# Optimization experiments

Hardware: AMD Instinct MI355X
Metric: run time of the kernel (lower is better)

Reference implementation:

```python
import jax, jax.numpy as jnp
import numpy as np

N_Q = 10000
B, S = 128, 200
M = 50          # memory_size
DK = 64         # memory_key_state_dim == q_embed_dim == final_fc_dim
DV = 128        # memory_value_state_dim == qa_embed_dim
F = 64          # final_fc_dim


def setup_inputs() -> dict:
    key = jax.random.key(0)
    ks = jax.random.split(key, 14)
    q_data = jax.random.randint(ks[0], (B, S), 0, N_Q + 1)
    qa_data = jax.random.randint(ks[1], (B, S), 0, 2 * N_Q + 1)
    # target in {-1 (pad), 0, 1}
    target = jax.random.randint(ks[2], (B, S), -1, 2).astype(jnp.float32)
    q_embed_w = jax.random.normal(ks[3], (N_Q + 1, DK), jnp.float32) * 0.1
    q_embed_w = q_embed_w.at[0].set(0.0)  # padding_idx=0
    qa_embed_w = jax.random.normal(ks[4], (2 * N_Q + 1, DV), jnp.float32) * 0.1
    qa_embed_w = qa_embed_w.at[0].set(0.0)
    mem_key = jax.random.normal(ks[5], (M, DK), jnp.float32) * (2.0 / DK) ** 0.5
    init_mem_value = jax.random.normal(ks[6], (M, DV), jnp.float32) * (2.0 / DV) ** 0.5
    erase_w = jax.random.normal(ks[7], (DV, DV), jnp.float32) * (2.0 / DV) ** 0.5
    erase_b = jnp.zeros((DV,), jnp.float32)
    add_w = jax.random.normal(ks[8], (DV, DV), jnp.float32) * (2.0 / DV) ** 0.5
    add_b = jnp.zeros((DV,), jnp.float32)
    read_w = jax.random.normal(ks[9], (F, DV + F), jnp.float32) * (2.0 / (DV + F)) ** 0.5
    read_b = jnp.zeros((F,), jnp.float32)
    pred_w = jax.random.normal(ks[10], (1, F), jnp.float32) * (2.0 / F) ** 0.5
    pred_b = jnp.zeros((1,), jnp.float32)
    return {
        'q_data': q_data, 'qa_data': qa_data, 'target': target,
        'q_embed_w': q_embed_w, 'qa_embed_w': qa_embed_w,
        'mem_key': mem_key, 'init_mem_value': init_mem_value,
        'erase_w': erase_w, 'erase_b': erase_b,
        'add_w': add_w, 'add_b': add_b,
        'read_w': read_w, 'read_b': read_b,
        'pred_w': pred_w, 'pred_b': pred_b,
    }


def reference(q_data, qa_data, target, q_embed_w, qa_embed_w, mem_key,
              init_mem_value, erase_w, erase_b, add_w, add_b,
              read_w, read_b, pred_w, pred_b):
    q_e = q_embed_w[q_data]    # [B,S,DK]
    qa_e = qa_embed_w[qa_data]  # [B,S,DV]
    Mv0 = jnp.broadcast_to(init_mem_value, (q_data.shape[0],) + init_mem_value.shape)  # [B,M,DV]

    def step(Mv, x):
        q, qa = x                                           # [B,DK], [B,DV]
        w = jax.nn.softmax(q @ mem_key.T, axis=1)           # addressing -> [B,M]
        read = jnp.einsum('bm,bmv->bv', w, Mv)              # weighted read (before write)
        e = jax.nn.sigmoid(qa @ erase_w.T + erase_b)        # [B,DV]
        a = jnp.tanh(qa @ add_w.T + add_b)                  # [B,DV]
        Mv_new = Mv * (1.0 - w[:, :, None] * e[:, None, :]) + w[:, :, None] * a[:, None, :]
        return Mv_new, read

    _, reads = jax.lax.scan(step, Mv0, (q_e.transpose(1, 0, 2), qa_e.transpose(1, 0, 2)))
    reads = reads.transpose(1, 0, 2)                        # [B,S,DV]

    h = jnp.tanh(jnp.concatenate([reads, q_e], axis=-1) @ read_w.T + read_b)  # [B,S,F]
    logits = (h @ pred_w.T + pred_b)[..., 0]                # [B,S]

    mask = target >= 0
    t = jnp.where(mask, target, 0.0)
    # stable BCE with logits
    bce = jnp.maximum(logits, 0.0) - logits * t + jnp.log1p(jnp.exp(-jnp.abs(logits)))
    n_valid = jnp.maximum(jnp.sum(mask.astype(jnp.float32)), 1.0)
    loss = jnp.sum(jnp.where(mask, bce, 0.0)) / n_valid
    probs = jnp.where(mask, jax.nn.sigmoid(logits), 0.0)    # masked predictions, fixed shape
    return loss, probs
```

## Files before the change

kernel.cpp:

```cpp
#include <hip/hip_runtime.h>
#include <math.h>

#define BB 128
#define SS 200
#define MM 50
#define DKK 64
#define DVV 128
#define FF 64
#define NROW (BB*SS)

#define WROW 64
#define NFCB (NROW/64)
#define WLDS 136
#define FLDS 200
#define CLEN 25
#define MP 25
#define NSCB 100

#define W_OFF   0L
#define EA_OFF  (W_OFF + (long)NROW*WROW)
#define R_OFF   (EA_OFF + (long)NROW*DVV*2)
#define ACC_OFF (R_OFF + (long)NROW*DVV)

typedef __attribute__((ext_vector_type(8))) short bf16x8;
typedef __attribute__((ext_vector_type(4))) float f32x4;
typedef __attribute__((ext_vector_type(2))) float f32x2;

__device__ __forceinline__ short f2bf(float f) {
    unsigned u = __builtin_bit_cast(unsigned, f);
    u += 0x7fff + ((u >> 16) & 1);
    return (short)(u >> 16);
}
__device__ __forceinline__ bf16x8 cvt8(const float* p) {
    float4 lo = *(const float4*)p;
    float4 hi = *(const float4*)(p + 4);
    bf16x8 f;
    f[0] = f2bf(lo.x); f[1] = f2bf(lo.y); f[2] = f2bf(lo.z); f[3] = f2bf(lo.w);
    f[4] = f2bf(hi.x); f[5] = f2bf(hi.y); f[6] = f2bf(hi.z); f[7] = f2bf(hi.w);
    return f;
}

__global__ __launch_bounds__(256) void k_pre(const int* __restrict__ q_data,
                                             const float* __restrict__ q_embed_w,
                                             const float* __restrict__ mem_key,
                                             const int* __restrict__ qa_data,
                                             const float* __restrict__ qa_embed_w,
                                             const float* __restrict__ erase_w,
                                             const float* __restrict__ erase_b,
                                             const float* __restrict__ add_w,
                                             const float* __restrict__ add_b,
                                             float* __restrict__ w_out,
                                             float* __restrict__ EA,
                                             float* __restrict__ acc) {
    __shared__ union {
        short  wl[2 * 128 * WLDS];
        float4 mk[MM * 16];
    } sh;
    int tid = threadIdx.x;
    int bid = blockIdx.x;

    if (bid < NSCB) {
        if (bid == 0 && tid == 0) {
            acc[0] = 0.f; acc[1] = 0.f;
            ((unsigned*)acc)[2] = 0u;
        }
        const float4* mkg = (const float4*)mem_key;
        for (int i = tid; i < MM * 16; i += 256) sh.mk[i] = mkg[i];
        __syncthreads();

        int item = bid * 256 + tid;
        int qidx = q_data[item];
        const float4* qg = (const float4*)(q_embed_w + (long)qidx * DKK);
        float4 q[16];
#pragma unroll
        for (int i = 0; i < 16; i++) q[i] = qg[i];

        float s[MM];
        float mx = -1e30f;
#pragma unroll 2
        for (int m = 0; m < MM; m++) {
            float a = 0.f;
#pragma unroll
            for (int k4 = 0; k4 < 16; k4++) {
                float4 mkv = sh.mk[m * 16 + k4];
                float4 qv = q[k4];
                a = fmaf(qv.x, mkv.x, a);
                a = fmaf(qv.y, mkv.y, a);
                a = fmaf(qv.z, mkv.z, a);
                a = fmaf(qv.w, mkv.w, a);
            }
            s[m] = a;
            mx = fmaxf(mx, a);
        }
        float sum = 0.f;
#pragma unroll
        for (int m = 0; m < MM; m++) { s[m] = expf(s[m] - mx); sum += s[m]; }
        float inv = 1.f / sum;

        float* wo = w_out + (long)item * WROW;
#pragma unroll
        for (int m = 0; m < MM; m++) wo[m] = s[m] * inv;
#pragma unroll
        for (int m = MM; m < WROW; m++) wo[m] = 0.f;
        return;
    }

    int r0 = (bid - NSCB) * 64;
    int lane = tid & 63;
    int wv = tid >> 6;
    int n = lane & 15;
    int quad = lane >> 4;

    for (int i = tid; i < 8192; i += 256) {
        int mat = i >> 12;
        int r = (i >> 5) & 127;
        int p = i & 31;
        float4 src = *(const float4*)((mat ? add_w : erase_w) + r * 128 + p * 4);
        short4 d;
        d.x = f2bf(src.x); d.y = f2bf(src.y); d.z = f2bf(src.z); d.w = f2bf(src.w);
        *(short4*)(sh.wl + (mat * 128 + r) * WLDS + p * 4) = d;
    }

    int arow = r0 + wv * 16 + n;
    int qidx = qa_data[arow];
    const float* qp = qa_embed_w + (long)qidx * DVV + quad * 8;
    bf16x8 afrag[4];
#pragma unroll
    for (int kb = 0; kb < 4; kb++) afrag[kb] = cvt8(qp + kb * 32);

    float eb_[8], ab_[8];
#pragma unroll
    for (int vt = 0; vt < 8; vt++) {
        eb_[vt] = erase_b[vt * 16 + n];
        ab_[vt] = add_b[vt * 16 + n];
    }
    __syncthreads();

    int rowbase = r0 + wv * 16 + quad * 4;
#pragma unroll 2
    for (int vt = 0; vt < 8; vt++) {
        int vrow = vt * 16 + n;
        f32x4 ae = {0.f, 0.f, 0.f, 0.f};
        f32x4 aa = {0.f, 0.f, 0.f, 0.f};
#pragma unroll
        for (int kb = 0; kb < 4; kb++) {
            bf16x8 be = *(const bf16x8*)(sh.wl + vrow * WLDS + kb * 32 + quad * 8);
            bf16x8 ba = *(const bf16x8*)(sh.wl + (128 + vrow) * WLDS + kb * 32 + quad * 8);
            ae = __builtin_amdgcn_mfma_f32_16x16x32_bf16(afrag[kb], be, ae, 0, 0, 0);
            aa = __builtin_amdgcn_mfma_f32_16x16x32_bf16(afrag[kb], ba, aa, 0, 0, 0);
        }
        int v = vt * 16 + n;
        float eb = eb_[vt], ab = ab_[vt];
#pragma unroll
        for (int r = 0; r < 4; r++) {
            float ev = 1.f / (1.f + __expf(-(ae[r] + eb)));
            float av = 2.f / (1.f + __expf(-2.f * (aa[r] + ab))) - 1.f;
            float2 o; o.x = ev; o.y = av;
            *(float2*)(EA + (((long)(rowbase + r)) * DVV + v) * 2) = o;
        }
    }
}

__device__ __forceinline__ void scan_pass1(const float4* __restrict__ wq,
                                           const float* __restrict__ eab,
                                           f32x2* A2, f32x2* B2) {
    const f32x2 one = {1.f, 1.f};
    float2 e0 = *(const float2*)eab;
    float2 e1 = *(const float2*)(eab + (long)1 * DVV * 2);
#pragma unroll 1
    for (int t = 0; t < CLEN; t++) {
        int tp = (t + 2 < CLEN) ? t + 2 : CLEN - 1;
        float2 en = *(const float2*)(eab + (long)tp * DVV * 2);
        f32x2 ne2 = {-e0.x, -e0.x};
        f32x2 a2  = {e0.y, e0.y};
#pragma unroll
        for (int c = 0; c < 13; c++) {
            float4 q = wq[t * 16 + c];
            {
                int j = 2 * c;
                f32x2 w2 = {q.x, q.y};
                f32x2 al = w2 * ne2 + one;
                A2[j] = A2[j] * al;
                B2[j] = al * B2[j] + w2 * a2;
            }
            if (c < 12) {
                int j = 2 * c + 1;
                f32x2 w2 = {q.z, q.w};
                f32x2 al = w2 * ne2 + one;
                A2[j] = A2[j] * al;
                B2[j] = al * B2[j] + w2 * a2;
            }
        }
        e0 = e1; e1 = en;
    }
}

__device__ __forceinline__ void scan_pass2(const float4* __restrict__ wq,
                                           const float* __restrict__ eab,
                                           float* __restrict__ Rb,
                                           f32x2* Mv) {
    float2 e0 = *(const float2*)eab;
    float2 e1 = *(const float2*)(eab + (long)1 * DVV * 2);
#pragma unroll 1
    for (int t = 0; t < CLEN; t++) {
        int tp = (t + 2 < CLEN) ? t + 2 : CLEN - 1;
        float2 en = *(const float2*)(eab + (long)tp * DVV * 2);
        f32x2 ne2 = {-e0.x, -e0.x};
        f32x2 a2  = {e0.y, e0.y};
        f32x2 rd  = {0.f, 0.f};
#pragma unroll
        for (int c = 0; c < 13; c++) {
            float4 q = wq[t * 16 + c];
            {
                int j = 2 * c;
                f32x2 w2 = {q.x, q.y};
                rd = rd + w2 * Mv[j];
                f32x2 s = ne2 * Mv[j] + a2;
                Mv[j] = Mv[j] + w2 * s;
            }
            if (c < 12) {
                int j = 2 * c + 1;
                f32x2 w2 = {q.z, q.w};
                rd = rd + w2 * Mv[j];
                f32x2 s = ne2 * Mv[j] + a2;
                Mv[j] = Mv[j] + w2 * s;
            }
        }
        Rb[t * DVV] = rd.x + rd.y;
        e0 = e1; e1 = en;
    }
}

__global__ __launch_bounds__(512, 1) void k_scan(const float* __restrict__ w_pad,
                                                 const float* __restrict__ EA,
                                                 const float* __restrict__ init_mv,
                                                 float* __restrict__ R) {
    __shared__ float Wl[SS * WROW];
    __shared__ float Sb[MM * 64];
    int b   = blockIdx.x >> 1;
    int vh  = blockIdx.x & 1;
    int tid = threadIdx.x;
    int lane  = tid & 63;
    int chunk = tid >> 6;
    int v  = vh * 64 + lane;
    int t0 = chunk * CLEN;

    {
        const float4* wg = (const float4*)(w_pad + (long)b * SS * WROW);
        float4* wl4 = (float4*)Wl;
        for (int i = tid; i < SS * WROW / 4; i += 512) wl4[i] = wg[i];
    }
    __syncthreads();

    const float4* wq  = (const float4*)(Wl + t0 * WROW);
    const float*  eab = EA + (((long)b * SS + t0) * DVV + v) * 2;
    float*        Rb  = R + ((long)b * SS + t0) * DVV + v;

    const f32x2 one = {1.f, 1.f};
    f32x2 A2[MP], B2[MP];
    f32x2 Mv[MP];

    if (chunk == 0) {
#pragma unroll
        for (int j = 0; j < MP; j++) {
            Mv[j].x = init_mv[(2 * j) * DVV + v];
            Mv[j].y = init_mv[(2 * j + 1) * DVV + v];
        }
        scan_pass2(wq, eab, Rb, Mv);
#pragma unroll
        for (int j = 0; j < MP; j++) {
            Sb[(2 * j) * 64 + lane] = Mv[j].x;
            Sb[(2 * j + 1) * 64 + lane] = Mv[j].y;
        }
    } else if (chunk < 7) {
#pragma unroll
        for (int j = 0; j < MP; j++) { A2[j] = one; B2[j] = (f32x2){0.f, 0.f}; }
        scan_pass1(wq, eab, A2, B2);
    }
    __syncthreads();

    for (int c = 1; c < 8; c++) {
        if (chunk == c) {
#pragma unroll
            for (int j = 0; j < MP; j++) {
                Mv[j].x = Sb[(2 * j) * 64 + lane];
                Mv[j].y = Sb[(2 * j + 1) * 64 + lane];
            }
            if (c < 7) {
#pragma unroll
                for (int j = 0; j < MP; j++) {
                    f32x2 nb = A2[j] * Mv[j] + B2[j];
                    Sb[(2 * j) * 64 + lane] = nb.x;
                    Sb[(2 * j + 1) * 64 + lane] = nb.y;
                }
            }
        }
        __syncthreads();
    }

    if (chunk > 0) scan_pass2(wq, eab, Rb, Mv);
}

__global__ __launch_bounds__(256) void k_fc(const float* __restrict__ Rr,
                                            const int* __restrict__ q_data,
                                            const float* __restrict__ q_embed_w,
                                            const float* __restrict__ read_w,
                                            const float* __restrict__ read_b,
                                            const float* __restrict__ pred_w,
                                            const float* __restrict__ pred_b,
                                            const float* __restrict__ target,
                                            float* __restrict__ out,
                                            float* __restrict__ acc) {
    __shared__ short Wl[64 * FLDS];
    __shared__ float2 red[4];
    int tid = threadIdx.x;
    int r0 = blockIdx.x * 64;
    int lane = tid & 63;
    int wv = tid >> 6;
    int n = lane & 15;
    int quad = lane >> 4;

    for (int i = tid; i < 3072; i += 256) {
        int f = i / 48, p = i - f * 48;
        float4 src = *(const float4*)(read_w + f * 192 + p * 4);
        short4 d;
        d.x = f2bf(src.x); d.y = f2bf(src.y); d.z = f2bf(src.z); d.w = f2bf(src.w);
        *(short4*)(Wl + f * FLDS + p * 4) = d;
    }

    int arow = r0 + wv * 16 + n;
    const float* rp = Rr + (long)arow * DVV + quad * 8;
    int qi = q_data[arow];
    const float* qp = q_embed_w + (long)qi * DKK + quad * 8;
    bf16x8 afrag[6];
#pragma unroll
    for (int kb = 0; kb < 4; kb++) afrag[kb] = cvt8(rp + kb * 32);
#pragma unroll
    for (int kb = 0; kb < 2; kb++) afrag[4 + kb] = cvt8(qp + kb * 32);

    float rb_[4], pw_[4];
#pragma unroll
    for (int ft = 0; ft < 4; ft++) {
        rb_[ft] = read_b[ft * 16 + n];
        pw_[ft] = pred_w[ft * 16 + n];
    }
    float pb = pred_b[0];
    __syncthreads();

    int rowbase = r0 + wv * 16 + quad * 4;
    float pv[4] = {0.f, 0.f, 0.f, 0.f};
#pragma unroll
    for (int ft = 0; ft < 4; ft++) {
        int f = ft * 16 + n;
        f32x4 ac = {0.f, 0.f, 0.f, 0.f};
#pragma unroll
        for (int kb = 0; kb < 6; kb++) {
            bf16x8 bfr = *(const bf16x8*)(Wl + f * FLDS + kb * 32 + quad * 8);
            ac = __builtin_amdgcn_mfma_f32_16x16x32_bf16(afrag[kb], bfr, ac, 0, 0, 0);
        }
        float rb = rb_[ft], pw = pw_[ft];
#pragma unroll
        for (int r = 0; r < 4; r++) {
            float h = 2.f / (1.f + __expf(-2.f * (ac[r] + rb))) - 1.f;
            pv[r] = fmaf(pw, h, pv[r]);
        }
    }

    float bce_sum = 0.f, cnt = 0.f;
#pragma unroll
    for (int r = 0; r < 4; r++) {
        float p = pv[r];
        p += __shfl_xor(p, 1, 64);
        p += __shfl_xor(p, 2, 64);
        p += __shfl_xor(p, 4, 64);
        p += __shfl_xor(p, 8, 64);
        if (n == 0) {
            int row = rowbase + r;
            float tgt = target[row];
            float logit = p + pb;
            float prob = 0.f;
            if (tgt >= 0.f) {
                prob = 1.f / (1.f + __expf(-logit));
                float bce = fmaxf(logit, 0.f) - logit * tgt + log1pf(__expf(-fabsf(logit)));
                bce_sum += bce;
                cnt += 1.f;
            }
            out[1 + row] = prob;
        }
    }
    bce_sum += __shfl_xor(bce_sum, 16, 64);
    bce_sum += __shfl_xor(bce_sum, 32, 64);
    cnt     += __shfl_xor(cnt, 16, 64);
    cnt     += __shfl_xor(cnt, 32, 64);
    if (lane == 0) { red[wv].x = bce_sum; red[wv].y = cnt; }
    __syncthreads();
    if (tid == 0) {
        float bsum = red[0].x + red[1].x + red[2].x + red[3].x;
        float csum = red[0].y + red[1].y + red[2].y + red[3].y;
        atomicAdd(&acc[0], bsum);
        atomicAdd(&acc[1], csum);
        __threadfence();
        unsigned prev = atomicAdd((unsigned*)acc + 2, 1u);
        if (prev == NFCB - 1) {
            __threadfence();
            float B = atomicAdd(&acc[0], 0.f);
            float C = atomicAdd(&acc[1], 0.f);
            out[0] = B / fmaxf(C, 1.f);
        }
    }
}

extern "C" void kernel_launch(void* const* d_in, const int* in_sizes, int n_in,
                              void* d_out, int out_size, void* d_ws, size_t ws_size,
                              hipStream_t stream) {
    const int*   q_data     = (const int*)d_in[0];
    const int*   qa_data    = (const int*)d_in[1];
    const float* target     = (const float*)d_in[2];
    const float* q_embed_w  = (const float*)d_in[3];
    const float* qa_embed_w = (const float*)d_in[4];
    const float* mem_key    = (const float*)d_in[5];
    const float* init_mv    = (const float*)d_in[6];
    const float* erase_w    = (const float*)d_in[7];
    const float* erase_b    = (const float*)d_in[8];
    const float* add_w      = (const float*)d_in[9];
    const float* add_b      = (const float*)d_in[10];
    const float* read_w     = (const float*)d_in[11];
    const float* read_b     = (const float*)d_in[12];
    const float* pred_w     = (const float*)d_in[13];
    const float* pred_b     = (const float*)d_in[14];
    float* out = (float*)d_out;
    float* ws  = (float*)d_ws;

    float* w_all = ws + W_OFF;
    float* EA    = ws + EA_OFF;
    float* R     = ws + R_OFF;
    float* acc   = ws + ACC_OFF;

    k_pre<<<NSCB + NROW / 64, 256, 0, stream>>>(q_data, q_embed_w, mem_key,
                                                qa_data, qa_embed_w,
                                                erase_w, erase_b, add_w, add_b,
                                                w_all, EA, acc);
    k_scan<<<BB * 2, 512, 0, stream>>>(w_all, EA, init_mv, R);
    k_fc<<<NFCB, 256, 0, stream>>>(R, q_data, q_embed_w, read_w, read_b,
                                   pred_w, pred_b, target, out, acc);
}
```

Before: 183.0 us.

## Split scan memory slots across half-waves to double block count

The scan kernel now splits the 50 memory slots between the two 32-lane halves of each wave. Each lane handles 13 slot pairs instead of 25, and the read is combined with a cross-lane shuffle. The grid doubles to four blocks per batch, each covering 32 value columns, and launch bounds allow two blocks per CU. This aims to raise parallelism and occupancy, and to cut per-thread register pressure and serial work in the latency-bound recurrence. In exchange it adds a shuffle per timestep, duplicate padding work on the last slot pair, and loads the shared W tile twice as many times overall.

```diff
diff --git a/kernel.cpp b/kernel.cpp
--- a/kernel.cpp
+++ b/kernel.cpp
@@ -14,7 +14,7 @@
 #define WLDS 136
 #define FLDS 200
 #define CLEN 25
-#define MP 25
+#define MPH 13
 #define NSCB 100
 
 #define W_OFF   0L
@@ -161,7 +161,7 @@
     }
 }
 
-__device__ __forceinline__ void scan_pass1(const float4* __restrict__ wq,
+__device__ __forceinline__ void scan_pass1(const float2* __restrict__ wp, int j0,
                                            const float* __restrict__ eab,
                                            f32x2* A2, f32x2* B2) {
     const f32x2 one = {1.f, 1.f};
@@ -174,30 +174,20 @@
         f32x2 ne2 = {-e0.x, -e0.x};
         f32x2 a2  = {e0.y, e0.y};
 #pragma unroll
-        for (int c = 0; c < 13; c++) {
-            float4 q = wq[t * 16 + c];
-            {
-                int j = 2 * c;
-                f32x2 w2 = {q.x, q.y};
-                f32x2 al = w2 * ne2 + one;
-                A2[j] = A2[j] * al;
-                B2[j] = al * B2[j] + w2 * a2;
-            }
-            if (c < 12) {
-                int j = 2 * c + 1;
-                f32x2 w2 = {q.z, q.w};
-                f32x2 al = w2 * ne2 + one;
-                A2[j] = A2[j] * al;
-                B2[j] = al * B2[j] + w2 * a2;
-            }
+        for (int j = 0; j < MPH; j++) {
+            float2 q = wp[t * 32 + j0 + j];
+            f32x2 w2 = {q.x, q.y};
+            f32x2 al = w2 * ne2 + one;
+            A2[j] = A2[j] * al;
+            B2[j] = al * B2[j] + w2 * a2;
         }
         e0 = e1; e1 = en;
     }
 }
 
-__device__ __forceinline__ void scan_pass2(const float4* __restrict__ wq,
+__device__ __forceinline__ void scan_pass2(const float2* __restrict__ wp, int j0,
                                            const float* __restrict__ eab,
-                                           float* __restrict__ Rb,
+                                           float* __restrict__ Rb, int mh,
                                            f32x2* Mv) {
     float2 e0 = *(const float2*)eab;
     float2 e1 = *(const float2*)(eab + (long)1 * DVV * 2);
@@ -209,40 +199,35 @@
         f32x2 a2  = {e0.y, e0.y};
         f32x2 rd  = {0.f, 0.f};
 #pragma unroll
-        for (int c = 0; c < 13; c++) {
-            float4 q = wq[t * 16 + c];
-            {
-                int j = 2 * c;
-                f32x2 w2 = {q.x, q.y};
-                rd = rd + w2 * Mv[j];
-                f32x2 s = ne2 * Mv[j] + a2;
-                Mv[j] = Mv[j] + w2 * s;
-            }
-            if (c < 12) {
-                int j = 2 * c + 1;
-                f32x2 w2 = {q.z, q.w};
-                rd = rd + w2 * Mv[j];
-                f32x2 s = ne2 * Mv[j] + a2;
-                Mv[j] = Mv[j] + w2 * s;
-            }
-        }
-        Rb[t * DVV] = rd.x + rd.y;
+        for (int j = 0; j < MPH; j++) {
+            float2 q = wp[t * 32 + j0 + j];
+            f32x2 w2 = {q.x, q.y};
+            rd = rd + w2 * Mv[j];
+            f32x2 s = ne2 * Mv[j] + a2;
+            Mv[j] = Mv[j] + w2 * s;
+        }
+        float r = rd.x + rd.y;
+        r += __shfl_xor(r, 32, 64);
+        if (mh == 0) Rb[t * DVV] = r;
         e0 = e1; e1 = en;
     }
 }
 
-__global__ __launch_bounds__(512, 1) void k_scan(const float* __restrict__ w_pad,
+__global__ __launch_bounds__(512, 2) void k_scan(const float* __restrict__ w_pad,
                                                  const float* __restrict__ EA,
                                                  const float* __restrict__ init_mv,
                                                  float* __restrict__ R) {
     __shared__ float Wl[SS * WROW];
-    __shared__ float Sb[MM * 64];
-    int b   = blockIdx.x >> 1;
-    int vh  = blockIdx.x & 1;
+    __shared__ float Sb[52 * 32];
+    int b   = blockIdx.x >> 2;
+    int vq  = blockIdx.x & 3;
     int tid = threadIdx.x;
     int lane  = tid & 63;
     int chunk = tid >> 6;
-    int v  = vh * 64 + lane;
+    int mh = lane >> 5;
+    int vl = lane & 31;
+    int v  = vq * 32 + vl;
+    int j0 = mh * MPH;
     int t0 = chunk * CLEN;
 
     {
@@ -252,53 +237,56 @@
     }
     __syncthreads();
 
-    const float4* wq  = (const float4*)(Wl + t0 * WROW);
+    const float2* wp  = (const float2*)(Wl + t0 * WROW);
     const float*  eab = EA + (((long)b * SS + t0) * DVV + v) * 2;
     float*        Rb  = R + ((long)b * SS + t0) * DVV + v;
 
     const f32x2 one = {1.f, 1.f};
-    f32x2 A2[MP], B2[MP];
-    f32x2 Mv[MP];
+    f32x2 A2[MPH], B2[MPH];
+    f32x2 Mv[MPH];
 
     if (chunk == 0) {
 #pragma unroll
-        for (int j = 0; j < MP; j++) {
-            Mv[j].x = init_mv[(2 * j) * DVV + v];
-            Mv[j].y = init_mv[(2 * j + 1) * DVV + v];
-        }
-        scan_pass2(wq, eab, Rb, Mv);
-#pragma unroll
-        for (int j = 0; j < MP; j++) {
-            Sb[(2 * j) * 64 + lane] = Mv[j].x;
-            Sb[(2 * j + 1) * 64 + lane] = Mv[j].y;
+        for (int j = 0; j < MPH; j++) {
+            int m0 = 2 * (j0 + j), m1 = m0 + 1;
+            if (m0 > MM - 2) m0 = MM - 2;
+            if (m1 > MM - 1) m1 = MM - 1;
+            Mv[j].x = init_mv[m0 * DVV + v];
+            Mv[j].y = init_mv[m1 * DVV + v];
+        }
+        scan_pass2(wp, j0, eab, Rb, mh, Mv);
+#pragma unroll
+        for (int j = 0; j < MPH; j++) {
+            Sb[(2 * (j0 + j)) * 32 + vl] = Mv[j].x;
+            Sb[(2 * (j0 + j) + 1) * 32 + vl] = Mv[j].y;
         }
     } else if (chunk < 7) {
 #pragma unroll
-        for (int j = 0; j < MP; j++) { A2[j] = one; B2[j] = (f32x2){0.f, 0.f}; }
-        scan_pass1(wq, eab, A2, B2);
+        for (int j = 0; j < MPH; j++) { A2[j] = one; B2[j] = (f32x2){0.f, 0.f}; }
+        scan_pass1(wp, j0, eab, A2, B2);
     }
     __syncthreads();
 
     for (int c = 1; c < 8; c++) {
         if (chunk == c) {
 #pragma unroll
-            for (int j = 0; j < MP; j++) {
-                Mv[j].x = Sb[(2 * j) * 64 + lane];
-                Mv[j].y = Sb[(2 * j + 1) * 64 + lane];
+            for (int j = 0; j < MPH; j++) {
+                Mv[j].x = Sb[(2 * (j0 + j)) * 32 + vl];
+                Mv[j].y = Sb[(2 * (j0 + j) + 1) * 32 + vl];
             }
             if (c < 7) {
 #pragma unroll
-                for (int j = 0; j < MP; j++) {
+                for (int j = 0; j < MPH; j++) {
                     f32x2 nb = A2[j] * Mv[j] + B2[j];
-                    Sb[(2 * j) * 64 + lane] = nb.x;
-                    Sb[(2 * j + 1) * 64 + lane] = nb.y;
+                    Sb[(2 * (j0 + j)) * 32 + vl] = nb.x;
+                    Sb[(2 * (j0 + j) + 1) * 32 + vl] = nb.y;
                 }
             }
         }
         __syncthreads();
     }
 
-    if (chunk > 0) scan_pass2(wq, eab, Rb, Mv);
+    if (chunk > 0) scan_pass2(wp, j0, eab, Rb, mh, Mv);
 }
 
 __global__ __launch_bounds__(256) void k_fc(const float* __restrict__ Rr,
@@ -440,7 +428,7 @@
                                                 qa_data, qa_embed_w,
                                                 erase_w, erase_b, add_w, add_b,
                                                 w_all, EA, acc);
-    k_scan<<<BB * 2, 512, 0, stream>>>(w_all, EA, init_mv, R);
+    k_scan<<<BB * 4, 512, 0, stream>>>(w_all, EA, init_mv, R);
     k_fc<<<NFCB, 256, 0, stream>>>(R, q_data, q_embed_w, read_w, read_b,
                                    pred_w, pred_b, target, out, acc);
 }
```

New measurement: 174.5 us. 1.05x faster.
